# Kernel optimization log

Hardware: AMD Instinct MI355X
Metric: run time of the kernel (lower is better)

## Reference

```python
import jax, jax.numpy as jnp
import numpy as np


def setup_inputs() -> dict:
    key = jax.random.key(0)
    x = jax.random.normal(key, (2, 2048, 512), dtype=jnp.float32)
    return {"x": x, "num_heads": 8, "kernel_size": 63}


def reference(x, num_heads, kernel_size):
    # NATTEN na1d with dilation=1: each query attends to a kernel_size window
    # centered at its position; near the sequence edges the window is shifted
    # (clamped) to stay fully inside [0, L), so every query sees exactly K keys.
    B, L, D = x.shape
    H = num_heads
    hd = D // H
    K = kernel_size
    scale = float(hd) ** -0.5

    qkv = x.reshape(B, L, H, hd)  # q == k == v == reshaped x

    # window start per query position, clamped so the window fits in bounds
    start = jnp.clip(jnp.arange(L) - K // 2, 0, L - K)          # (L,)
    idx = start[:, None] + jnp.arange(K)                         # (L, K)

    kv = qkv[:, idx]                                             # (B, L, K, H, hd)
    scores = jnp.einsum("blhd,blkhd->bhlk", qkv, kv) * scale     # (B, H, L, K)
    attn = jax.nn.softmax(scores, axis=-1)
    out = jnp.einsum("bhlk,blkhd->blhd", attn, kv)               # (B, L, H, hd)
    return out.reshape(B, L, D)
```

## Files before the change

kernel.cpp:

```cpp
#include <hip/hip_runtime.h>

#define B_ 2
#define L_ 2048
#define H_ 8
#define HD 64
#define K_ 63
#define TQ 64
#define NT (L_ / TQ)
#define ROWS 128
#define EXPC 0.1803368801111204f

typedef __attribute__((ext_vector_type(8))) short bf16x8;
typedef __attribute__((ext_vector_type(4))) float f32x4;

__device__ inline unsigned cvt_pk_bf16(float lo, float hi) {
    unsigned r;
    asm("v_cvt_pk_bf16_f32 %0, %1, %2" : "=v"(r) : "v"(lo), "v"(hi));
    return r;
}

__global__ __launch_bounds__(256, 2) void natten1d_mfma(
    const float* __restrict__ x, float* __restrict__ out)
{
    __shared__ unsigned short kv_sh [ROWS * 64];
    __shared__ unsigned short kvT_sh[64 * ROWS];
    __shared__ unsigned short pt_sh [4 * 16 * 128];

    const int bid = blockIdx.x;
    const int wid = (bid & 7) * (B_ * H_ * NT / 8) + (bid >> 3);
    const int bh  = wid / NT;
    const int t   = wid % NT;
    const int b   = bh / H_;
    const int h   = bh % H_;
    const int l0  = t * TQ;
    const int key_base = min(max(l0 - K_ / 2, 0), L_ - K_);
    const int qoff     = l0 - key_base;

    const int tid = threadIdx.x;
    const int d4  = tid & 15;
    const int rg0 = tid >> 4;

    const float4* xb = (const float4*)x + (size_t)b * (L_ * H_ * HD / 4) + h * (HD / 4);
    float4 ld[8];
    #pragma unroll
    for (int m = 0; m < 2; ++m) {
        const int rg = rg0 + m * 16;
        #pragma unroll
        for (int rr = 0; rr < 4; ++rr) {
            const int g = key_base + rg * 4 + rr;
            ld[m * 4 + rr] = (g < L_) ? xb[(size_t)g * (H_ * HD / 4) + d4]
                                      : make_float4(0.f, 0.f, 0.f, 0.f);
        }
    }
    #pragma unroll
    for (int m = 0; m < 2; ++m) {
        const int rg = rg0 + m * 16;
        #pragma unroll
        for (int rr = 0; rr < 4; ++rr) {
            const int r = rg * 4 + rr;
            const float4 v = ld[m * 4 + rr];
            uint2 w;
            w.x = cvt_pk_bf16(v.x, v.y);
            w.y = cvt_pk_bf16(v.z, v.w);
            *(uint2*)&kv_sh[r * 64 + (((d4 >> 1) ^ (r & 7)) << 3) + (d4 & 1) * 4] = w;
        }
        #pragma unroll
        for (int e = 0; e < 4; ++e) {
            const int d = d4 * 4 + e;
            const float* f0 = (const float*)&ld[m * 4 + 0];
            const float* f1 = (const float*)&ld[m * 4 + 1];
            const float* f2 = (const float*)&ld[m * 4 + 2];
            const float* f3 = (const float*)&ld[m * 4 + 3];
            uint2 w;
            w.x = cvt_pk_bf16(f0[e], f1[e]);
            w.y = cvt_pk_bf16(f2[e], f3[e]);
            *(uint2*)&kvT_sh[d * 128 + (((rg >> 1) ^ (d & 15)) << 3) + ((rg & 1) << 2)] = w;
        }
    }
    __syncthreads();

    const int wave = tid >> 6;
    const int lane = tid & 63;
    const int lq = lane & 15;
    const int lg = lane >> 4;

    const int q0    = wave * 16;
    const int soff0 = min(max(l0 + q0 - K_ / 2, 0), L_ - K_) - key_base;
    const int wb    = min(soff0 & ~15, ROWS - 96);
    const int qrow  = qoff + q0 + lq;
    const int soffq = min(max(l0 + q0 + lq - K_ / 2, 0), L_ - K_) - key_base;
    const int cbase = wb + lg * 4 - soffq;

    bf16x8 bq[2];
    bq[0] = *(const bf16x8*)&kv_sh[qrow * 64 + ((lg ^ (qrow & 7)) << 3)];
    bq[1] = *(const bf16x8*)&kv_sh[qrow * 64 + (((4 + lg) ^ (qrow & 7)) << 3)];

    f32x4 acc[6];
    #pragma unroll
    for (int nb = 0; nb < 6; ++nb) acc[nb] = (f32x4){0.f, 0.f, 0.f, 0.f};
    #pragma unroll
    for (int nb = 0; nb < 6; ++nb) {
        const int krow = wb + nb * 16 + lq;
        const bf16x8 a0 = *(const bf16x8*)&kv_sh[krow * 64 + ((lg ^ (krow & 7)) << 3)];
        const bf16x8 a1 = *(const bf16x8*)&kv_sh[krow * 64 + (((4 + lg) ^ (krow & 7)) << 3)];
        acc[nb] = __builtin_amdgcn_mfma_f32_16x16x32_bf16(a0, bq[0], acc[nb], 0, 0, 0);
        acc[nb] = __builtin_amdgcn_mfma_f32_16x16x32_bf16(a1, bq[1], acc[nb], 0, 0, 0);
    }

    float mx = -1e30f;
    #pragma unroll
    for (int nb = 0; nb < 6; ++nb) {
        #pragma unroll
        for (int r = 0; r < 4; ++r) {
            const bool valid = (unsigned)(cbase + nb * 16 + r) < (unsigned)K_;
            const float s = valid ? acc[nb][r] : -1e30f;
            acc[nb][r] = s;
            mx = fmaxf(mx, s);
        }
    }
    mx = fmaxf(mx, __shfl_xor(mx, 16));
    mx = fmaxf(mx, __shfl_xor(mx, 32));
    float z = 0.f;
    #pragma unroll
    for (int nb = 0; nb < 6; ++nb) {
        #pragma unroll
        for (int r = 0; r < 4; ++r) {
            const float e = exp2f((acc[nb][r] - mx) * EXPC);
            acc[nb][r] = e;
            z += e;
        }
    }
    z += __shfl_xor(z, 16);
    z += __shfl_xor(z, 32);
    const float rz = 1.0f / z;

    unsigned short* ptw = &pt_sh[wave * 16 * 128];
    #pragma unroll
    for (int nb = 0; nb < 6; ++nb) {
        uint2 w;
        w.x = cvt_pk_bf16(acc[nb][0] * rz, acc[nb][1] * rz);
        w.y = cvt_pk_bf16(acc[nb][2] * rz, acc[nb][3] * rz);
        const int g = nb * 2 + (lg >> 1);
        *(uint2*)&ptw[lq * 128 + ((g ^ lq) << 3) + ((lg & 1) << 2)] = w;
    }

    bf16x8 ap[3];
    #pragma unroll
    for (int kc = 0; kc < 3; ++kc)
        ap[kc] = *(const bf16x8*)&ptw[lq * 128 + (((kc * 4 + lg) ^ lq) << 3)];
    f32x4 o4[4];
    #pragma unroll
    for (int nb = 0; nb < 4; ++nb) o4[nb] = (f32x4){0.f, 0.f, 0.f, 0.f};
    const int kg0 = wb >> 3;
    #pragma unroll
    for (int nb = 0; nb < 4; ++nb) {
        const int d = nb * 16 + lq;
        #pragma unroll
        for (int kc = 0; kc < 3; ++kc) {
            const bf16x8 bv =
                *(const bf16x8*)&kvT_sh[d * 128 + (((kg0 + kc * 4 + lg) ^ (d & 15)) << 3)];
            o4[nb] = __builtin_amdgcn_mfma_f32_16x16x32_bf16(ap[kc], bv, o4[nb], 0, 0, 0);
        }
    }

    #pragma unroll
    for (int nb = 0; nb < 4; ++nb) {
        const int d = nb * 16 + lq;
        #pragma unroll
        for (int r = 0; r < 4; ++r) {
            const int q = q0 + lg * 4 + r;
            out[((size_t)(b * L_ + l0 + q) * H_ + h) * HD + d] = o4[nb][r];
        }
    }
}

extern "C" void kernel_launch(void* const* d_in, const int* in_sizes, int n_in,
                              void* d_out, int out_size, void* d_ws, size_t ws_size,
                              hipStream_t stream)
{
    const float* x = (const float*)d_in[0];
    float* out = (float*)d_out;
    natten1d_mfma<<<dim3(B_ * H_ * NT), dim3(256), 0, stream>>>(x, out);
}
```

Measured before the change: 11.15 us.

## Split head-dim staging into two halves to overlap second half with QK MFMAs

Each thread now loads one row-group across both head-dim halves. It converts and stores the first 32 dims to shared memory, runs the first QK^T MFMA pass on them, and only then converts and stores the second half, followed by another barrier and the second MFMA pass. The aim is to hide the LDS conversion and store latency of the second half behind the first half's matrix work. In exchange it adds a barrier and keeps the second-half registers live for longer, and all global loads are still issued up front.

```diff
diff --git a/kernel.cpp b/kernel.cpp
--- a/kernel.cpp
+++ b/kernel.cpp
@@ -37,44 +37,41 @@
     const int qoff     = l0 - key_base;
 
     const int tid = threadIdx.x;
-    const int d4  = tid & 15;
-    const int rg0 = tid >> 4;
+    const int c   = tid & 7;
+    const int rw  = tid >> 3;
 
     const float4* xb = (const float4*)x + (size_t)b * (L_ * H_ * HD / 4) + h * (HD / 4);
-    float4 ld[8];
-    #pragma unroll
-    for (int m = 0; m < 2; ++m) {
-        const int rg = rg0 + m * 16;
-        #pragma unroll
-        for (int rr = 0; rr < 4; ++rr) {
-            const int g = key_base + rg * 4 + rr;
-            ld[m * 4 + rr] = (g < L_) ? xb[(size_t)g * (H_ * HD / 4) + d4]
-                                      : make_float4(0.f, 0.f, 0.f, 0.f);
-        }
-    }
-    #pragma unroll
-    for (int m = 0; m < 2; ++m) {
-        const int rg = rg0 + m * 16;
-        #pragma unroll
-        for (int rr = 0; rr < 4; ++rr) {
-            const int r = rg * 4 + rr;
-            const float4 v = ld[m * 4 + rr];
-            uint2 w;
-            w.x = cvt_pk_bf16(v.x, v.y);
-            w.y = cvt_pk_bf16(v.z, v.w);
-            *(uint2*)&kv_sh[r * 64 + (((d4 >> 1) ^ (r & 7)) << 3) + (d4 & 1) * 4] = w;
-        }
+    float4 la[4], lb[4];
+    #pragma unroll
+    for (int rr = 0; rr < 4; ++rr) {
+        const int g = key_base + rw * 4 + rr;
+        const bool ok = (g < L_);
+        const size_t ro = (size_t)g * (H_ * HD / 4);
+        la[rr] = ok ? xb[ro + c]     : make_float4(0.f, 0.f, 0.f, 0.f);
+        lb[rr] = ok ? xb[ro + c + 8] : make_float4(0.f, 0.f, 0.f, 0.f);
+    }
+
+    #pragma unroll
+    for (int rr = 0; rr < 4; ++rr) {
+        const int r = rw * 4 + rr;
+        uint2 w;
+        w.x = cvt_pk_bf16(la[rr].x, la[rr].y);
+        w.y = cvt_pk_bf16(la[rr].z, la[rr].w);
+        *(uint2*)&kv_sh[r * 64 + (((c >> 1) ^ (r & 7)) << 3) + (c & 1) * 4] = w;
+    }
+    {
+        const int key = rw * 4;
+        const float* f0 = (const float*)&la[0];
+        const float* f1 = (const float*)&la[1];
+        const float* f2 = (const float*)&la[2];
+        const float* f3 = (const float*)&la[3];
         #pragma unroll
         for (int e = 0; e < 4; ++e) {
-            const int d = d4 * 4 + e;
-            const float* f0 = (const float*)&ld[m * 4 + 0];
-            const float* f1 = (const float*)&ld[m * 4 + 1];
-            const float* f2 = (const float*)&ld[m * 4 + 2];
-            const float* f3 = (const float*)&ld[m * 4 + 3];
+            const int d = c * 4 + e;
             uint2 w;
             w.x = cvt_pk_bf16(f0[e], f1[e]);
             w.y = cvt_pk_bf16(f2[e], f3[e]);
-            *(uint2*)&kvT_sh[d * 128 + (((rg >> 1) ^ (d & 15)) << 3) + ((rg & 1) << 2)] = w;
+            *(uint2*)&kvT_sh[d * 128 + (((key >> 3) ^ (d & 15)) << 3) + (key & 7)] = w;
         }
     }
     __syncthreads();
@@ -91,20 +88,52 @@
     const int soffq = min(max(l0 + q0 + lq - K_ / 2, 0), L_ - K_) - key_base;
     const int cbase = wb + lg * 4 - soffq;
 
-    bf16x8 bq[2];
-    bq[0] = *(const bf16x8*)&kv_sh[qrow * 64 + ((lg ^ (qrow & 7)) << 3)];
-    bq[1] = *(const bf16x8*)&kv_sh[qrow * 64 + (((4 + lg) ^ (qrow & 7)) << 3)];
-
     f32x4 acc[6];
     #pragma unroll
     for (int nb = 0; nb < 6; ++nb) acc[nb] = (f32x4){0.f, 0.f, 0.f, 0.f};
-    #pragma unroll
-    for (int nb = 0; nb < 6; ++nb) {
-        const int krow = wb + nb * 16 + lq;
-        const bf16x8 a0 = *(const bf16x8*)&kv_sh[krow * 64 + ((lg ^ (krow & 7)) << 3)];
-        const bf16x8 a1 = *(const bf16x8*)&kv_sh[krow * 64 + (((4 + lg) ^ (krow & 7)) << 3)];
-        acc[nb] = __builtin_amdgcn_mfma_f32_16x16x32_bf16(a0, bq[0], acc[nb], 0, 0, 0);
-        acc[nb] = __builtin_amdgcn_mfma_f32_16x16x32_bf16(a1, bq[1], acc[nb], 0, 0, 0);
+    {
+        const bf16x8 bq0 = *(const bf16x8*)&kv_sh[qrow * 64 + ((lg ^ (qrow & 7)) << 3)];
+        #pragma unroll
+        for (int nb = 0; nb < 6; ++nb) {
+            const int krow = wb + nb * 16 + lq;
+            const bf16x8 a0 = *(const bf16x8*)&kv_sh[krow * 64 + ((lg ^ (krow & 7)) << 3)];
+            acc[nb] = __builtin_amdgcn_mfma_f32_16x16x32_bf16(a0, bq0, acc[nb], 0, 0, 0);
+        }
+    }
+
+    #pragma unroll
+    for (int rr = 0; rr < 4; ++rr) {
+        const int r = rw * 4 + rr;
+        uint2 w;
+        w.x = cvt_pk_bf16(lb[rr].x, lb[rr].y);
+        w.y = cvt_pk_bf16(lb[rr].z, lb[rr].w);
+        *(uint2*)&kv_sh[r * 64 + ((((c >> 1) + 4) ^ (r & 7)) << 3) + (c & 1) * 4] = w;
+    }
+    {
+        const int key = rw * 4;
+        const float* f0 = (const float*)&lb[0];
+        const float* f1 = (const float*)&lb[1];
+        const float* f2 = (const float*)&lb[2];
+        const float* f3 = (const float*)&lb[3];
+        #pragma unroll
+        for (int e = 0; e < 4; ++e) {
+            const int d = 32 + c * 4 + e;
+            uint2 w;
+            w.x = cvt_pk_bf16(f0[e], f1[e]);
+            w.y = cvt_pk_bf16(f2[e], f3[e]);
+            *(uint2*)&kvT_sh[d * 128 + (((key >> 3) ^ (d & 15)) << 3) + (key & 7)] = w;
+        }
+    }
+    __syncthreads();
+
+    {
+        const bf16x8 bq1 = *(const bf16x8*)&kv_sh[qrow * 64 + (((4 + lg) ^ (qrow & 7)) << 3)];
+        #pragma unroll
+        for (int nb = 0; nb < 6; ++nb) {
+            const int krow = wb + nb * 16 + lq;
+            const bf16x8 a1 = *(const bf16x8*)&kv_sh[krow * 64 + (((4 + lg) ^ (krow & 7)) << 3)];
+            acc[nb] = __builtin_amdgcn_mfma_f32_16x16x32_bf16(a1, bq1, acc[nb], 0, 0, 0);
+        }
     }
 
     float mx = -1e30f;
```

New measurement: 10.65 us. -4.5%, faster.
